# Kernel tuning notes

Hardware: AMD Instinct MI355X
Metric: run time of the kernel (lower is better)

Reference implementation:

```python
import jax, jax.numpy as jnp
import numpy as np

B, H, W = 4, 112, 112
N = H * W              # 12544 tokens
NBHD = 48              # local neighborhood size
DIM = 256
OUT_DIM = 512
INNER = 4              # inner_ch of weight_net
TABLE = 4096           # pre_table rows
ALPHA = 4.0
DS_RATE = 0.25
STRIDE = 2
RESERVE = (H // 4) * (W // 4)  # 784 reserve tokens (pos % 4 == 0)
EPS = 1e-5


def _ln(x, g, b):
    m = x.mean(-1, keepdims=True)
    v = ((x - m) ** 2).mean(-1, keepdims=True)
    return (x - m) / jnp.sqrt(v + EPS) * g + b


def setup_inputs() -> dict:
    key = jax.random.key(0)
    ks = jax.random.split(key, 8)
    ii, jj = jnp.meshgrid(jnp.arange(H), jnp.arange(W), indexing='ij')
    pos = jnp.stack([ii, jj], -1).reshape(1, N, 2).astype(jnp.float32)
    pos = jnp.tile(pos, (B, 1, 1))                             # b x n x 2 integer grid
    feat = jax.random.normal(ks[0], (B, N, DIM), jnp.float32)
    member_idx = jax.random.randint(ks[1], (B, N, NBHD), 0, N)
    cluster_mask = (jax.random.uniform(ks[2], (B, N, NBHD)) > 0.1).astype(jnp.float32)
    learned_prob = jax.random.uniform(ks[3], (B, N, 1), dtype=jnp.float32)
    pe_idx = jax.random.randint(ks[4], (B, N, NBHD), 0, TABLE)
    pre_table = jax.random.normal(ks[5], (TABLE, 5), jnp.float32)
    w1 = jax.random.normal(ks[6], (5, INNER), jnp.float32) * 0.4
    b1 = jnp.zeros((INNER,), jnp.float32)
    ln1_g = jnp.ones((INNER,), jnp.float32)
    ln1_b = jnp.zeros((INNER,), jnp.float32)
    norm_g = jnp.ones((INNER * DIM,), jnp.float32)
    norm_b = jnp.zeros((INNER * DIM,), jnp.float32)
    lin_w = jax.random.normal(ks[7], (INNER * DIM, OUT_DIM), jnp.float32) * (1.0 / np.sqrt(INNER * DIM))
    lin_b = jnp.zeros((OUT_DIM,), jnp.float32)
    return dict(pos=pos, feat=feat, member_idx=member_idx, cluster_mask=cluster_mask,
                learned_prob=learned_prob, stride=STRIDE, pe_idx=pe_idx, reserve_num=RESERVE,
                pre_table=pre_table, w1=w1, b1=b1, ln1_g=ln1_g, ln1_b=ln1_b,
                norm_g=norm_g, norm_b=norm_b, lin_w=lin_w, lin_b=lin_b)


def reference(pos, feat, member_idx, cluster_mask, learned_prob, stride, pe_idx,
              reserve_num, pre_table, w1, b1, ln1_g, ln1_b, norm_g, norm_b, lin_w, lin_b):
    b, n, c = feat.shape
    keep_num = int(n * DS_RATE)
    pos_long = pos.astype(jnp.int32)
    # stride == 2 branch: tokens on the coarse grid get prob 1
    grid_prob = jnp.all(pos_long % stride == 0, axis=-1).astype(jnp.float32)      # b x n
    lp_s = jax.lax.stop_gradient(learned_prob).reshape(b, n) * ALPHA              # detached scores
    final_prob = grid_prob + lp_s
    reserve_mask = jnp.all(pos_long % (stride * 2) == 0, axis=-1).astype(jnp.float32)
    final_prob = final_prob + reserve_mask * (-100.0)
    sample_num = keep_num - reserve_num
    _, sample_idx = jax.lax.top_k(final_prob, sample_num)                         # b x sample_num
    # per-row nonzero of reserve_mask (exactly reserve_num hits per row)
    flat_nz = jnp.nonzero(reserve_mask.reshape(-1) > 0, size=b * reserve_num)[0]
    reserve_idx = (flat_nz % n).reshape(b, reserve_num).astype(sample_idx.dtype)
    idx = jnp.concatenate([sample_idx, reserve_idx], axis=1)                      # b x keep_num

    pos_k = jnp.take_along_axis(pos, idx[:, :, None], axis=1)                     # b x keep x 2
    nbhd = member_idx.shape[-1]
    mem_k = jnp.take_along_axis(member_idx, idx[:, :, None], axis=1)              # b x keep x nbhd
    pe_k = jnp.take_along_axis(pe_idx, idx[:, :, None], axis=1)
    cm_k = jnp.take_along_axis(cluster_mask, idx[:, :, None], axis=1)
    lp = jnp.take_along_axis(learned_prob, mem_k.reshape(b, -1, 1), axis=1)
    lp = lp.reshape(b, keep_num, nbhd, 1)

    # weight_net on the small PE table, then gather per-edge weights
    wt = jax.nn.gelu(_ln(pre_table @ w1 + b1, ln1_g, ln1_b), approximate=False)   # TABLE x INNER
    weights = wt[pe_k]                                                            # b x keep x nbhd x INNER
    weights = weights * (lp * cm_k[..., None])

    # CLUSTENWF: gather neighbor features and weighted-sum over the neighborhood
    gathered = jnp.take_along_axis(feat, mem_k.reshape(b, -1, 1), axis=1)
    gathered = gathered.reshape(b, keep_num, nbhd, c)                             # b x keep x nbhd x c
    out = jnp.einsum('bnkm,bnkc->bnmc', weights, gathered).reshape(b, keep_num, INNER * c)
    out = _ln(out, norm_g, norm_b)
    return pos_k, out @ lin_w + lin_b
```

## Files before the change

### kernel.cpp

```cpp
#include <hip/hip_runtime.h>

typedef unsigned short u16;
typedef unsigned int u32;
typedef unsigned long long u64;

#define NB 4
#define NTOK 12544
#define NBHD 48
#define DIM 256
#define OUTD 512
#define KEEPN 3136
#define SAMPLEN 2352
#define RESN 784
#define GW 112
#define TABLE 4096
#define POSN (NB * KEEPN * 2)
#define QTR (NTOK / 4)
#define NBKT 16384

#define BLKM 128
#define BLKN 256
#define BROW 40

#define FEATB_BYTES (25690112ull)
#define XWS_BYTES   (25690112ull)
#define LINT_BYTES  (1048576ull)
#define KEYS_BYTES  (401408ull)
#define PART_BYTES  (802816ull)
#define WS_NEED (FEATB_BYTES + XWS_BYTES + LINT_BYTES + KEYS_BYTES + PART_BYTES)

__device__ __forceinline__ float bf2f(u16 u) {
    union { u32 i; float f; } v; v.i = ((u32)u) << 16; return v.f;
}
__device__ __forceinline__ float asf(u32 u) {
    union { u32 i; float f; } v; v.i = u; return v.f;
}
__device__ __forceinline__ u16 f2bf(float f) {
    union { u32 i; float f; } v; v.f = f;
    return (u16)((v.i + 0x7FFFu + ((v.i >> 16) & 1u)) >> 16);
}

typedef __bf16 bf16x8 __attribute__((ext_vector_type(8)));
typedef float floatx4 __attribute__((ext_vector_type(4)));
typedef float floatx2 __attribute__((ext_vector_type(2)));

__device__ __forceinline__ float make_f(float lp, int n) {
    int i = n / GW, j = n % GW;
    float f = lp * 4.0f;
    if (((i | j) & 1) == 0) f = 1.0f + f;
    if (((i | j) & 3) == 0) f = f + (-100.0f);
    return f;
}
__device__ __forceinline__ u64 f_to_key(float f, int n) {
    union { float f; u32 u; } v; v.f = f;
    u32 m = (v.u & 0x80000000u) ? ~v.u : (v.u | 0x80000000u);
    return (((u64)m) << 32) | (u64)(0xFFFFFFFFu - (u32)n);
}
__device__ __forceinline__ int f_to_bucket(float f) {
    int b = (int)floorf(f * 3276.8f);
    return b < 0 ? 0 : (b > NBKT - 1 ? NBKT - 1 : b);
}

__global__ __launch_bounds__(256) void prep_kernel(
    const float* __restrict__ feat, u16* __restrict__ featb,
    const float* __restrict__ lin_w, u16* __restrict__ linT,
    u32* __restrict__ hist,
    const float* __restrict__ pre_table, const float* __restrict__ w1,
    const float* __restrict__ b1, const float* __restrict__ g1,
    const float* __restrict__ bb1, float* __restrict__ wt) {
    __shared__ u16 T[64 * 65];
    int bid = blockIdx.x;
    int t = threadIdx.x;
    if (bid >= 128) {
        int ft = (bid - 128) * 256 + t;
        float4 v = ((const float4*)feat)[ft];
        u64 w = (u64)f2bf(v.x) | ((u64)f2bf(v.y) << 16) |
                ((u64)f2bf(v.z) << 32) | ((u64)f2bf(v.w) << 48);
        ((u64*)featb)[ft] = w;
        return;
    }
    int bx = bid & 15, by = bid >> 4;
    int k0 = bx * 64, n0 = by * 64;
    hist[bid * 512 + t] = 0;
    hist[bid * 512 + 256 + t] = 0;
    int gid = bid * 256 + t;
    if (gid < TABLE) {
        float z[4];
#pragma unroll
        for (int m = 0; m < 4; ++m) {
            float acc = b1[m];
#pragma unroll
            for (int d = 0; d < 5; ++d) acc += pre_table[gid * 5 + d] * w1[d * 4 + m];
            z[m] = acc;
        }
        float mean = (z[0] + z[1] + z[2] + z[3]) * 0.25f;
        float var = 0.0f;
#pragma unroll
        for (int m = 0; m < 4; ++m) { float d = z[m] - mean; var += d * d; }
        float rstd = rsqrtf(var * 0.25f + 1e-5f);
        float wv[4];
#pragma unroll
        for (int m = 0; m < 4; ++m) {
            float y = (z[m] - mean) * rstd * g1[m] + bb1[m];
            wv[m] = 0.5f * y * (1.0f + erff(y * 0.70710678118654752f));
        }
        *(float4*)&wt[gid * 4] = make_float4(wv[0], wv[1], wv[2], wv[3]);
    }
    int r = t >> 2, c4 = (t & 3) * 16;
#pragma unroll
    for (int i = 0; i < 4; ++i) {
        float4 v = *(const float4*)&lin_w[(size_t)(k0 + r) * OUTD + n0 + c4 + i * 4];
        T[(c4 + i * 4 + 0) * 65 + r] = f2bf(v.x);
        T[(c4 + i * 4 + 1) * 65 + r] = f2bf(v.y);
        T[(c4 + i * 4 + 2) * 65 + r] = f2bf(v.z);
        T[(c4 + i * 4 + 3) * 65 + r] = f2bf(v.w);
    }
    __syncthreads();
    int nl = t >> 2, kc = (t & 3) * 16;
    union { uint4 v[2]; u16 h[16]; } u;
#pragma unroll
    for (int i = 0; i < 16; ++i) u.h[i] = T[nl * 65 + kc + i];
    u16* dst = &linT[(size_t)(n0 + nl) * 1024 + k0 + kc];
    *(uint4*)(dst + 0) = u.v[0];
    *(uint4*)(dst + 8) = u.v[1];
}

__global__ __launch_bounds__(256) void hist_kernel(
    const float* __restrict__ lprob, u32* __restrict__ hist) {
    int g = blockIdx.x * 256 + threadIdx.x;
    int b = g / NTOK, n = g % NTOK;
    int bkt = f_to_bucket(make_f(lprob[g], n));
    atomicAdd(&hist[b * NBKT + bkt], 1u);
}

__global__ __launch_bounds__(1024) void prefix_kernel(
    const u32* __restrict__ hist, u32* __restrict__ base, u32* __restrict__ cursor) {
    int b = blockIdx.x, t = threadIdx.x;
    const u32* h = hist + b * NBKT;
    u32 loc[16], own = 0;
#pragma unroll
    for (int i = 0; i < 16; ++i) { loc[i] = h[t * 16 + i]; own += loc[i]; }
    __shared__ u32 buf[2][1024];
    buf[0][t] = own;
    __syncthreads();
    int src = 0;
    for (int off = 1; off < 1024; off <<= 1) {
        u32 v = buf[src][t] + ((t + off < 1024) ? buf[src][t + off] : 0u);
        buf[src ^ 1][t] = v;
        src ^= 1;
        __syncthreads();
    }
    u32 above = buf[src][t] - own;
    u32 suf = 0, bout[16];
    for (int i = 15; i >= 0; --i) { bout[i] = above + suf; suf += loc[i]; }
    u32* bb = base + b * NBKT;
    u32* cc = cursor + b * NBKT;
#pragma unroll
    for (int i = 0; i < 16; ++i) { bb[t * 16 + i] = bout[i]; cc[t * 16 + i] = bout[i]; }
}

__global__ __launch_bounds__(256) void scatter_kernel(
    const float* __restrict__ lprob, u32* __restrict__ cursor,
    u64* __restrict__ slots) {
    int g = blockIdx.x * 256 + threadIdx.x;
    int b = g / NTOK, n = g % NTOK;
    float f = make_f(lprob[g], n);
    int bkt = f_to_bucket(f);
    u32 s = atomicAdd(&cursor[b * NBKT + bkt], 1u);
    slots[b * NTOK + s] = f_to_key(f, n);
}

__global__ __launch_bounds__(256) void rank_finalize_kernel(
    const float* __restrict__ lprob, const u32* __restrict__ hist,
    const u32* __restrict__ base, const u64* __restrict__ slots,
    float* __restrict__ pos_out) {
    int g = blockIdx.x * 256 + threadIdx.x;
    int b = g / NTOK, n = g % NTOK;
    int i = n / GW, j = n % GW;
    if (((i | j) & 3) == 0) {
        int r = (i >> 2) * 28 + (j >> 2);
        int slot = b * KEEPN + SAMPLEN + r;
        pos_out[slot * 2 + 0] = (float)i;
        pos_out[slot * 2 + 1] = (float)j;
        return;
    }
    float f = make_f(lprob[g], n);
    int bkt = f_to_bucket(f);
    u32 r0 = base[b * NBKT + bkt];
    if (r0 >= SAMPLEN) return;
    u64 my = f_to_key(f, n);
    u32 cnt = hist[b * NBKT + bkt];
    const u64* sl = slots + b * NTOK + r0;
    u32 rank = r0;
    for (u32 s = 0; s < cnt; ++s) rank += (sl[s] > my) ? 1u : 0u;
    if (rank < SAMPLEN) {
        int slot = b * KEEPN + (int)rank;
        pos_out[slot * 2 + 0] = (float)i;
        pos_out[slot * 2 + 1] = (float)j;
    }
}

__device__ __forceinline__ void consume8(uint2 d, float4 w,
                                         floatx2* accA, floatx2* accB) {
    floatx2 w01 = {w.x, w.y};
    floatx2 w23 = {w.z, w.w};
    float c0 = asf(d.x << 16);
    float c1 = asf(d.x & 0xFFFF0000u);
    float c2 = asf(d.y << 16);
    float c3 = asf(d.y & 0xFFFF0000u);
    floatx2 c0v = {c0, c0}, c1v = {c1, c1}, c2v = {c2, c2}, c3v = {c3, c3};
    accA[0] = __builtin_elementwise_fma(w01, c0v, accA[0]);
    accB[0] = __builtin_elementwise_fma(w23, c0v, accB[0]);
    accA[1] = __builtin_elementwise_fma(w01, c1v, accA[1]);
    accB[1] = __builtin_elementwise_fma(w23, c1v, accB[1]);
    accA[2] = __builtin_elementwise_fma(w01, c2v, accA[2]);
    accB[2] = __builtin_elementwise_fma(w23, c2v, accB[2]);
    accA[3] = __builtin_elementwise_fma(w01, c3v, accA[3]);
    accB[3] = __builtin_elementwise_fma(w23, c3v, accB[3]);
}

__global__ __launch_bounds__(256) void token_v8_kernel(
    const float* __restrict__ pos_in, u16* __restrict__ xdst,
    const int* __restrict__ member_idx, const int* __restrict__ pe_idx,
    const float* __restrict__ cmask, const float* __restrict__ lprob,
    const u16* __restrict__ featb, const float* __restrict__ wt,
    const float* __restrict__ norm_g, const float* __restrict__ norm_b) {
    int bi = blockIdx.x;
    int xcd = bi & 7, jj = bi >> 3;
    int b = xcd >> 1;
    int tid = threadIdx.x;
    int wave = tid >> 6, lane = tid & 63;
    int t = b * KEEPN + (xcd & 1) * 1568 + jj * 4 + wave;

    __shared__ float4 w_s[4][NBHD];

    float2 pp = *(const float2*)&pos_in[t * 2];
    int n_src = (int)pp.x * GW + (int)pp.y;

    u32 moffb = 0;
    if (lane < NBHD) {
        int e = (b * NTOK + n_src) * NBHD + lane;
        int mem = member_idx[e];
        float sc = lprob[b * NTOK + mem] * cmask[e];
        float4 w4 = *(const float4*)&wt[pe_idx[e] * 4];
        w_s[wave][lane] = make_float4(w4.x * sc, w4.y * sc, w4.z * sc, w4.w * sc);
        moffb = (u32)mem * (DIM * 2);
    }
    __syncthreads();

    floatx2 accA[4] = {};
    floatx2 accB[4] = {};
    const char* fb = (const char*)featb + (size_t)b * NTOK * DIM * 2;
    u32 lane8 = (u32)lane * 8;

#define GLD(dst, kk) { u32 mk = (u32)__builtin_amdgcn_readlane((int)moffb, (kk)); \
                       dst = *(const uint2*)(fb + mk + lane8); }
#pragma unroll
    for (int kb = 0; kb < NBHD; kb += 8) {
        uint2 d0, d1, d2, d3, d4, d5, d6, d7;
        GLD(d0, kb + 0); GLD(d1, kb + 1); GLD(d2, kb + 2); GLD(d3, kb + 3);
        GLD(d4, kb + 4); GLD(d5, kb + 5); GLD(d6, kb + 6); GLD(d7, kb + 7);
        consume8(d0, w_s[wave][kb + 0], accA, accB);
        consume8(d1, w_s[wave][kb + 1], accA, accB);
        consume8(d2, w_s[wave][kb + 2], accA, accB);
        consume8(d3, w_s[wave][kb + 3], accA, accB);
        consume8(d4, w_s[wave][kb + 4], accA, accB);
        consume8(d5, w_s[wave][kb + 5], accA, accB);
        consume8(d6, w_s[wave][kb + 6], accA, accB);
        consume8(d7, w_s[wave][kb + 7], accA, accB);
    }
#undef GLD

    float s1 = 0.0f, s2 = 0.0f;
#pragma unroll
    for (int j = 0; j < 4; ++j) {
        float v0 = accA[j][0], v1 = accA[j][1], v2 = accB[j][0], v3 = accB[j][1];
        s1 += v0 + v1 + v2 + v3;
        s2 += v0 * v0 + v1 * v1 + v2 * v2 + v3 * v3;
    }
#pragma unroll
    for (int off = 32; off > 0; off >>= 1) {
        s1 += __shfl_xor(s1, off, 64);
        s2 += __shfl_xor(s2, off, 64);
    }
    float mean = s1 * (1.0f / 1024.0f);
    float var = fmaxf(s2 * (1.0f / 1024.0f) - mean * mean, 0.0f);
    float rstd = rsqrtf(var + 1e-5f);

    u16* Xp = xdst + (size_t)t * 1024;
#pragma unroll
    for (int m = 0; m < 4; ++m) {
        int cc = m * 256 + lane * 4;
        float4 g4 = *(const float4*)&norm_g[cc];
        float4 b4 = *(const float4*)&norm_b[cc];
        float v0 = (m == 0) ? accA[0][0] : (m == 1) ? accA[0][1]
                 : (m == 2) ? accB[0][0] : accB[0][1];
        float v1 = (m == 0) ? accA[1][0] : (m == 1) ? accA[1][1]
                 : (m == 2) ? accB[1][0] : accB[1][1];
        float v2 = (m == 0) ? accA[2][0] : (m == 1) ? accA[2][1]
                 : (m == 2) ? accB[2][0] : accB[2][1];
        float v3 = (m == 0) ? accA[3][0] : (m == 1) ? accA[3][1]
                 : (m == 2) ? accB[3][0] : accB[3][1];
        u16 h0 = f2bf((v0 - mean) * rstd * g4.x + b4.x);
        u16 h1 = f2bf((v1 - mean) * rstd * g4.y + b4.y);
        u16 h2 = f2bf((v2 - mean) * rstd * g4.z + b4.z);
        u16 h3 = f2bf((v3 - mean) * rstd * g4.w + b4.w);
        u64 w = (u64)h0 | ((u64)h1 << 16) | ((u64)h2 << 32) | ((u64)h3 << 48);
        *(u64*)(Xp + cc) = w;
    }
}

#define GROW 40
__global__ __launch_bounds__(256) void gemm_tile_kernel(
    const u16* __restrict__ xws, const u16* __restrict__ linT,
    const float* __restrict__ lin_b, float* __restrict__ out) {
    __shared__ __align__(16) u16 As[128 * GROW];
    __shared__ __align__(16) u16 Bs[64 * GROW];
    int bid = blockIdx.x;
    int xcd = bid & 7, c = bid >> 3;
    int tile = xcd * 98 + c;
    int m0 = (tile >> 3) * 128, n0 = (tile & 7) * 64;

    int tid = threadIdx.x;
    int wave = tid >> 6, lane = tid & 63;
    int l15 = lane & 15, quad = lane >> 4;
    int wm = wave >> 1, wn = wave & 1;
    int sr = tid >> 2, sk = (tid & 3) * 8;

    const u16* Ap0 = xws + (size_t)(m0 + sr) * 1024 + sk;
    const u16* Ap1 = Ap0 + (size_t)64 * 1024;
    const u16* Bp0 = linT + (size_t)(n0 + sr) * 1024 + sk;

    uint4 a0 = *(const uint4*)(Ap0);
    uint4 a1 = *(const uint4*)(Ap1);
    uint4 b0 = *(const uint4*)(Bp0);

    floatx4 acc[4][2] = {};
    for (int kk = 0; kk < 1024; kk += 32) {
        __syncthreads();
        *(uint4*)&As[sr * GROW + sk] = a0;
        *(uint4*)&As[(64 + sr) * GROW + sk] = a1;
        *(uint4*)&Bs[sr * GROW + sk] = b0;
        __syncthreads();
        if (kk + 32 < 1024) {
            a0 = *(const uint4*)(Ap0 + kk + 32);
            a1 = *(const uint4*)(Ap1 + kk + 32);
            b0 = *(const uint4*)(Bp0 + kk + 32);
        }
        bf16x8 af[4], bfv[2];
#pragma unroll
        for (int mi = 0; mi < 4; ++mi)
            af[mi] = *(const bf16x8*)&As[(wm * 64 + mi * 16 + l15) * GROW + quad * 8];
#pragma unroll
        for (int ni = 0; ni < 2; ++ni)
            bfv[ni] = *(const bf16x8*)&Bs[(wn * 32 + ni * 16 + l15) * GROW + quad * 8];
#pragma unroll
        for (int mi = 0; mi < 4; ++mi)
#pragma unroll
            for (int ni = 0; ni < 2; ++ni)
                acc[mi][ni] = __builtin_amdgcn_mfma_f32_16x16x32_bf16(
                    af[mi], bfv[ni], acc[mi][ni], 0, 0, 0);
    }
#pragma unroll
    for (int ni = 0; ni < 2; ++ni) {
        int col = n0 + wn * 32 + ni * 16 + l15;
        float bias = lin_b[col];
#pragma unroll
        for (int mi = 0; mi < 4; ++mi)
#pragma unroll
            for (int reg = 0; reg < 4; ++reg) {
                int row = m0 + wm * 64 + mi * 16 + quad * 4 + reg;
                out[(size_t)row * OUTD + col] = acc[mi][ni][reg] + bias;
            }
    }
}

__global__ __launch_bounds__(256) void key_kernel(
    const float* __restrict__ lprob, u64* __restrict__ keys) {
    int g = blockIdx.x * 256 + threadIdx.x;
    int n = g % NTOK;
    keys[g] = f_to_key(make_f(lprob[g], n), n);
}

__global__ __launch_bounds__(256) void partial_rank_kernel(
    const u64* __restrict__ keys, u32* __restrict__ part) {
    int b = blockIdx.y, z = blockIdx.z;
    int n = blockIdx.x * 256 + threadIdx.x;
    u64 my = keys[b * NTOK + n];
    const u64* kb = keys + b * NTOK + z * QTR;
    u32 cnt = 0;
    for (int t = 0; t < QTR; t += 8) {
#pragma unroll
        for (int j = 0; j < 8; ++j) cnt += (kb[t + j] > my) ? 1u : 0u;
    }
    part[(z * NB + b) * NTOK + n] = cnt;
}

__global__ __launch_bounds__(256) void finalize_kernel(
    const u32* __restrict__ part, float* __restrict__ pos_out) {
    int b = blockIdx.y;
    int n = blockIdx.x * 256 + threadIdx.x;
    int g = b * NTOK + n;
    u32 rank = part[g] + part[(NB + b) * NTOK + n] +
               part[(2 * NB + b) * NTOK + n] + part[(3 * NB + b) * NTOK + n];
    int i = n / GW, j = n % GW;
    if (rank < SAMPLEN) {
        int slot = b * KEEPN + (int)rank;
        pos_out[slot * 2 + 0] = (float)i;
        pos_out[slot * 2 + 1] = (float)j;
    }
    if (((i | j) & 3) == 0) {
        int r = (i >> 2) * 28 + (j >> 2);
        int slot = b * KEEPN + SAMPLEN + r;
        pos_out[slot * 2 + 0] = (float)i;
        pos_out[slot * 2 + 1] = (float)j;
    }
}

__global__ __launch_bounds__(256) void token_fb_kernel(
    const float* __restrict__ pos_in, u16* __restrict__ xdst,
    const int* __restrict__ member_idx, const int* __restrict__ pe_idx,
    const float* __restrict__ cmask, const float* __restrict__ lprob,
    const float* __restrict__ featf, const float* __restrict__ pre_table,
    const float* __restrict__ w1, const float* __restrict__ b1,
    const float* __restrict__ g1, const float* __restrict__ bb1,
    const float* __restrict__ norm_g, const float* __restrict__ norm_b) {
    int t = blockIdx.x;
    int b = t / KEEPN;
    int tid = threadIdx.x;
    __shared__ int mem_s[NBHD];
    __shared__ float4 w_s[NBHD];
    __shared__ float red[10];

    int n_src = (int)pos_in[t * 2 + 0] * GW + (int)pos_in[t * 2 + 1];

    if (tid < NBHD) {
        int e = (b * NTOK + n_src) * NBHD + tid;
        int mem = member_idx[e];
        int pe = pe_idx[e];
        float cm = cmask[e];
        float lpe = lprob[b * NTOK + mem];
        float z[4];
#pragma unroll
        for (int m = 0; m < 4; ++m) {
            float acc = b1[m];
#pragma unroll
            for (int d = 0; d < 5; ++d) acc += pre_table[pe * 5 + d] * w1[d * 4 + m];
            z[m] = acc;
        }
        float mean = (z[0] + z[1] + z[2] + z[3]) * 0.25f;
        float var = 0.0f;
#pragma unroll
        for (int m = 0; m < 4; ++m) { float d = z[m] - mean; var += d * d; }
        float rstd = rsqrtf(var * 0.25f + 1e-5f);
        float sc = lpe * cm;
        float wv[4];
#pragma unroll
        for (int m = 0; m < 4; ++m) {
            float y = (z[m] - mean) * rstd * g1[m] + bb1[m];
            wv[m] = 0.5f * y * (1.0f + erff(y * 0.70710678118654752f)) * sc;
        }
        w_s[tid] = make_float4(wv[0], wv[1], wv[2], wv[3]);
        mem_s[tid] = mem;
    }
    __syncthreads();

    float a0 = 0.f, a1 = 0.f, a2 = 0.f, a3 = 0.f;
    size_t base = (size_t)b * NTOK * DIM + tid;
#pragma unroll 8
    for (int k = 0; k < NBHD; ++k) {
        float g = featf[base + (size_t)mem_s[k] * DIM];
        float4 w = w_s[k];
        a0 += w.x * g; a1 += w.y * g; a2 += w.z * g; a3 += w.w * g;
    }
    float s1 = a0 + a1 + a2 + a3;
    float s2 = a0 * a0 + a1 * a1 + a2 * a2 + a3 * a3;
#pragma unroll
    for (int off = 32; off > 0; off >>= 1) {
        s1 += __shfl_down(s1, off, 64);
        s2 += __shfl_down(s2, off, 64);
    }
    int wave = tid >> 6, lane = tid & 63;
    if (lane == 0) { red[wave] = s1; red[4 + wave] = s2; }
    __syncthreads();
    if (tid == 0) {
        float S = red[0] + red[1] + red[2] + red[3];
        float Q = red[4] + red[5] + red[6] + red[7];
        float mean = S * (1.0f / 1024.0f);
        float var = fmaxf(Q * (1.0f / 1024.0f) - mean * mean, 0.0f);
        red[8] = mean; red[9] = rsqrtf(var + 1e-5f);
    }
    __syncthreads();
    float mean = red[8], rstd = red[9];
    float acc4[4] = {a0, a1, a2, a3};
    u16* Xp = xdst + (size_t)t * 1024;
#pragma unroll
    for (int m = 0; m < 4; ++m) {
        int cc = m * 256 + tid;
        float v = (acc4[m] - mean) * rstd * norm_g[cc] + norm_b[cc];
        Xp[cc] = f2bf(v);
    }
}

__global__ __launch_bounds__(256) void gemm_inplace_kernel(
    const float* __restrict__ lin_w, const float* __restrict__ lin_b,
    float* __restrict__ out) {
    __shared__ __align__(16) u16 Bs[BLKN * BROW];
    int tile_m = blockIdx.x;
    int nblk = blockIdx.y;
    int tid = threadIdx.x;
    int wave = tid >> 6, lane = tid & 63;
    int l15 = lane & 15, quad = lane >> 4;

    const u16* Xbase = (const u16*)out;
    floatx4 acc[8][4] = {};

    for (int kk = 0; kk < 1024; kk += 32) {
        __syncthreads();
#pragma unroll
        for (int it = 0; it < 4; ++it) {
            int task = it * 256 + tid;
            int kp = task >> 6;
            int ng = task & 63;
            int k = kp * 2;
            int n0 = nblk * BLKN + ng * 4;
            float4 fa = *(const float4*)&lin_w[(size_t)(kk + k) * OUTD + n0];
            float4 fb = *(const float4*)&lin_w[(size_t)(kk + k + 1) * OUTD + n0];
            u16* bp = &Bs[(ng * 4) * BROW + k];
            *(u32*)(bp + 0 * BROW) = (u32)f2bf(fa.x) | ((u32)f2bf(fb.x) << 16);
            *(u32*)(bp + 1 * BROW) = (u32)f2bf(fa.y) | ((u32)f2bf(fb.y) << 16);
            *(u32*)(bp + 2 * BROW) = (u32)f2bf(fa.z) | ((u32)f2bf(fb.z) << 16);
            *(u32*)(bp + 3 * BROW) = (u32)f2bf(fa.w) | ((u32)f2bf(fb.w) << 16);
        }
        __syncthreads();
        bf16x8 bfrag[4];
#pragma unroll
        for (int ni = 0; ni < 4; ++ni)
            bfrag[ni] = *(const bf16x8*)&Bs[(wave * 64 + ni * 16 + l15) * BROW + quad * 8];
#pragma unroll
        for (int mi = 0; mi < 8; ++mi) {
            int row = tile_m * BLKM + mi * 16 + l15;
            bf16x8 af = *(const bf16x8*)&Xbase[(size_t)row * 1024 + kk + quad * 8];
#pragma unroll
            for (int ni = 0; ni < 4; ++ni)
                acc[mi][ni] = __builtin_amdgcn_mfma_f32_16x16x32_bf16(
                    af, bfrag[ni], acc[mi][ni], 0, 0, 0);
        }
    }
    __syncthreads();
#pragma unroll
    for (int mi = 0; mi < 8; ++mi)
#pragma unroll
        for (int ni = 0; ni < 4; ++ni) {
            int col = nblk * BLKN + wave * 64 + ni * 16 + l15;
            float bias = lin_b[col];
#pragma unroll
            for (int reg = 0; reg < 4; ++reg) {
                int row = tile_m * BLKM + mi * 16 + quad * 4 + reg;
                out[(size_t)row * OUTD + col] = acc[mi][ni][reg] + bias;
            }
        }
}

extern "C" void kernel_launch(void* const* d_in, const int* in_sizes, int n_in,
                              void* d_out, int out_size, void* d_ws, size_t ws_size,
                              hipStream_t stream) {
    const float* feat     = (const float*)d_in[1];
    const int* member_idx = (const int*)d_in[2];
    const float* cmask    = (const float*)d_in[3];
    const float* lprob    = (const float*)d_in[4];
    const int* pe_idx     = (const int*)d_in[6];
    const float* pre_table= (const float*)d_in[8];
    const float* w1       = (const float*)d_in[9];
    const float* b1       = (const float*)d_in[10];
    const float* g1       = (const float*)d_in[11];
    const float* bb1      = (const float*)d_in[12];
    const float* norm_g   = (const float*)d_in[13];
    const float* norm_b   = (const float*)d_in[14];
    const float* lin_w    = (const float*)d_in[15];
    const float* lin_b    = (const float*)d_in[16];

    float* pos_out = (float*)d_out;
    float* out     = pos_out + POSN;

    if (ws_size >= WS_NEED) {
        char* ws = (char*)d_ws;
        u16* featb = (u16*)ws;
        u16* xws   = (u16*)(ws + FEATB_BYTES);
        u16* linT  = (u16*)(ws + FEATB_BYTES + XWS_BYTES);
        u64* slots = (u64*)(ws + FEATB_BYTES + XWS_BYTES + LINT_BYTES);
        u32* hist  = (u32*)(ws + FEATB_BYTES + XWS_BYTES + LINT_BYTES + KEYS_BYTES);
        u32* base  = hist + NB * NBKT;
        u32* curs  = base + NB * NBKT;
        float* wtbuf = out;

        prep_kernel<<<12672, 256, 0, stream>>>(
            feat, featb, lin_w, linT, hist, pre_table, w1, b1, g1, bb1, wtbuf);
        hist_kernel<<<(NB * NTOK) / 256, 256, 0, stream>>>(lprob, hist);
        prefix_kernel<<<NB, 1024, 0, stream>>>(hist, base, curs);
        scatter_kernel<<<(NB * NTOK) / 256, 256, 0, stream>>>(lprob, curs, slots);
        rank_finalize_kernel<<<(NB * NTOK) / 256, 256, 0, stream>>>(
            lprob, hist, base, slots, pos_out);
        token_v8_kernel<<<(NB * KEEPN) / 4, 256, 0, stream>>>(
            pos_out, xws, member_idx, pe_idx, cmask, lprob, featb,
            wtbuf, norm_g, norm_b);
        gemm_tile_kernel<<<784, 256, 0, stream>>>(xws, linT, lin_b, out);
    } else {
        u64* keys = (u64*)out;
        u32* part = (u32*)((char*)out + 401408);

        key_kernel<<<(NB * NTOK) / 256, 256, 0, stream>>>(lprob, keys);
        partial_rank_kernel<<<dim3(49, NB, 4), 256, 0, stream>>>(keys, part);
        finalize_kernel<<<dim3(49, NB), 256, 0, stream>>>(part, pos_out);
        token_fb_kernel<<<NB * KEEPN, 256, 0, stream>>>(
            pos_out, (u16*)out, member_idx, pe_idx, cmask, lprob, feat,
            pre_table, w1, b1, g1, bb1, norm_g, norm_b);
        gemm_inplace_kernel<<<dim3(98, 2), 256, 0, stream>>>(lin_w, lin_b, out);
    }
}
```

Baseline: 238.4 us.

## Split neighborhood across half-waves with 16-byte gathers and LDS offsets

```diff
diff --git a/kernel.cpp b/kernel.cpp
--- a/kernel.cpp
+++ b/kernel.cpp
@@ -200,26 +200,24 @@
     }
 }
 
-__device__ __forceinline__ void consume8(uint2 d, float4 w,
-                                         floatx2* accA, floatx2* accB) {
+__device__ __forceinline__ void consume16(uint4 d, float4 w,
+                                          floatx2* accA, floatx2* accB) {
     floatx2 w01 = {w.x, w.y};
     floatx2 w23 = {w.z, w.w};
-    float c0 = asf(d.x << 16);
-    float c1 = asf(d.x & 0xFFFF0000u);
-    float c2 = asf(d.y << 16);
-    float c3 = asf(d.y & 0xFFFF0000u);
-    floatx2 c0v = {c0, c0}, c1v = {c1, c1}, c2v = {c2, c2}, c3v = {c3, c3};
-    accA[0] = __builtin_elementwise_fma(w01, c0v, accA[0]);
-    accB[0] = __builtin_elementwise_fma(w23, c0v, accB[0]);
-    accA[1] = __builtin_elementwise_fma(w01, c1v, accA[1]);
-    accB[1] = __builtin_elementwise_fma(w23, c1v, accB[1]);
-    accA[2] = __builtin_elementwise_fma(w01, c2v, accA[2]);
-    accB[2] = __builtin_elementwise_fma(w23, c2v, accB[2]);
-    accA[3] = __builtin_elementwise_fma(w01, c3v, accA[3]);
-    accB[3] = __builtin_elementwise_fma(w23, c3v, accB[3]);
-}
-
-__global__ __launch_bounds__(256) void token_v8_kernel(
+    float c[8];
+    c[0] = asf(d.x << 16); c[1] = asf(d.x & 0xFFFF0000u);
+    c[2] = asf(d.y << 16); c[3] = asf(d.y & 0xFFFF0000u);
+    c[4] = asf(d.z << 16); c[5] = asf(d.z & 0xFFFF0000u);
+    c[6] = asf(d.w << 16); c[7] = asf(d.w & 0xFFFF0000u);
+#pragma unroll
+    for (int j = 0; j < 8; ++j) {
+        floatx2 cs = {c[j], c[j]};
+        accA[j] = __builtin_elementwise_fma(w01, cs, accA[j]);
+        accB[j] = __builtin_elementwise_fma(w23, cs, accB[j]);
+    }
+}
+
+__global__ __launch_bounds__(256) void token_v9_kernel(
     const float* __restrict__ pos_in, u16* __restrict__ xdst,
     const int* __restrict__ member_idx, const int* __restrict__ pe_idx,
     const float* __restrict__ cmask, const float* __restrict__ lprob,
@@ -232,48 +230,56 @@
     int wave = tid >> 6, lane = tid & 63;
     int t = b * KEEPN + (xcd & 1) * 1568 + jj * 4 + wave;
 
-    __shared__ float4 w_s[4][NBHD];
+    __shared__ __align__(16) float4 w_s[4][NBHD];
+    __shared__ __align__(16) int moff_s[4][NBHD];
 
     float2 pp = *(const float2*)&pos_in[t * 2];
     int n_src = (int)pp.x * GW + (int)pp.y;
 
-    u32 moffb = 0;
     if (lane < NBHD) {
         int e = (b * NTOK + n_src) * NBHD + lane;
         int mem = member_idx[e];
         float sc = lprob[b * NTOK + mem] * cmask[e];
         float4 w4 = *(const float4*)&wt[pe_idx[e] * 4];
-        w_s[wave][lane] = make_float4(w4.x * sc, w4.y * sc, w4.z * sc, w4.w * sc);
-        moffb = (u32)mem * (DIM * 2);
+        int slot = (lane & 1) * 24 + (lane >> 1);
+        w_s[wave][slot] = make_float4(w4.x * sc, w4.y * sc, w4.z * sc, w4.w * sc);
+        moff_s[wave][slot] = mem * (DIM * 2);
     }
     __syncthreads();
 
-    floatx2 accA[4] = {};
-    floatx2 accB[4] = {};
+    int half = lane >> 5;
+    int l5 = lane & 31;
+    u32 l16 = (u32)l5 * 16;
     const char* fb = (const char*)featb + (size_t)b * NTOK * DIM * 2;
-    u32 lane8 = (u32)lane * 8;
-
-#define GLD(dst, kk) { u32 mk = (u32)__builtin_amdgcn_readlane((int)moffb, (kk)); \
-                       dst = *(const uint2*)(fb + mk + lane8); }
-#pragma unroll
-    for (int kb = 0; kb < NBHD; kb += 8) {
-        uint2 d0, d1, d2, d3, d4, d5, d6, d7;
-        GLD(d0, kb + 0); GLD(d1, kb + 1); GLD(d2, kb + 2); GLD(d3, kb + 3);
-        GLD(d4, kb + 4); GLD(d5, kb + 5); GLD(d6, kb + 6); GLD(d7, kb + 7);
-        consume8(d0, w_s[wave][kb + 0], accA, accB);
-        consume8(d1, w_s[wave][kb + 1], accA, accB);
-        consume8(d2, w_s[wave][kb + 2], accA, accB);
-        consume8(d3, w_s[wave][kb + 3], accA, accB);
-        consume8(d4, w_s[wave][kb + 4], accA, accB);
-        consume8(d5, w_s[wave][kb + 5], accA, accB);
-        consume8(d6, w_s[wave][kb + 6], accA, accB);
-        consume8(d7, w_s[wave][kb + 7], accA, accB);
-    }
-#undef GLD
+    const int* obase = &moff_s[wave][half * 24];
+    const float4* wbase = &w_s[wave][half * 24];
+
+    floatx2 accA[8] = {};
+    floatx2 accB[8] = {};
+#pragma unroll
+    for (int pb = 0; pb < 6; ++pb) {
+        int4 o = *(const int4*)(obase + pb * 4);
+        uint4 e0 = *(const uint4*)(fb + (u32)o.x + l16);
+        uint4 e1 = *(const uint4*)(fb + (u32)o.y + l16);
+        uint4 e2 = *(const uint4*)(fb + (u32)o.z + l16);
+        uint4 e3 = *(const uint4*)(fb + (u32)o.w + l16);
+        consume16(e0, wbase[pb * 4 + 0], accA, accB);
+        consume16(e1, wbase[pb * 4 + 1], accA, accB);
+        consume16(e2, wbase[pb * 4 + 2], accA, accB);
+        consume16(e3, wbase[pb * 4 + 3], accA, accB);
+    }
+
+#pragma unroll
+    for (int j = 0; j < 8; ++j) {
+        accA[j][0] += __shfl_xor(accA[j][0], 32, 64);
+        accA[j][1] += __shfl_xor(accA[j][1], 32, 64);
+        accB[j][0] += __shfl_xor(accB[j][0], 32, 64);
+        accB[j][1] += __shfl_xor(accB[j][1], 32, 64);
+    }
 
     float s1 = 0.0f, s2 = 0.0f;
 #pragma unroll
-    for (int j = 0; j < 4; ++j) {
+    for (int j = 0; j < 8; ++j) {
         float v0 = accA[j][0], v1 = accA[j][1], v2 = accB[j][0], v3 = accB[j][1];
         s1 += v0 + v1 + v2 + v3;
         s2 += v0 * v0 + v1 * v1 + v2 * v2 + v3 * v3;
@@ -283,30 +289,42 @@
         s1 += __shfl_xor(s1, off, 64);
         s2 += __shfl_xor(s2, off, 64);
     }
-    float mean = s1 * (1.0f / 1024.0f);
-    float var = fmaxf(s2 * (1.0f / 1024.0f) - mean * mean, 0.0f);
+    float mean = s1 * (1.0f / 2048.0f);
+    float var = fmaxf(s2 * (1.0f / 2048.0f) - mean * mean, 0.0f);
     float rstd = rsqrtf(var + 1e-5f);
 
     u16* Xp = xdst + (size_t)t * 1024;
-#pragma unroll
-    for (int m = 0; m < 4; ++m) {
-        int cc = m * 256 + lane * 4;
-        float4 g4 = *(const float4*)&norm_g[cc];
-        float4 b4 = *(const float4*)&norm_b[cc];
-        float v0 = (m == 0) ? accA[0][0] : (m == 1) ? accA[0][1]
-                 : (m == 2) ? accB[0][0] : accB[0][1];
-        float v1 = (m == 0) ? accA[1][0] : (m == 1) ? accA[1][1]
-                 : (m == 2) ? accB[1][0] : accB[1][1];
-        float v2 = (m == 0) ? accA[2][0] : (m == 1) ? accA[2][1]
-                 : (m == 2) ? accB[2][0] : accB[2][1];
-        float v3 = (m == 0) ? accA[3][0] : (m == 1) ? accA[3][1]
-                 : (m == 2) ? accB[3][0] : accB[3][1];
-        u16 h0 = f2bf((v0 - mean) * rstd * g4.x + b4.x);
-        u16 h1 = f2bf((v1 - mean) * rstd * g4.y + b4.y);
-        u16 h2 = f2bf((v2 - mean) * rstd * g4.z + b4.z);
-        u16 h3 = f2bf((v3 - mean) * rstd * g4.w + b4.w);
-        u64 w = (u64)h0 | ((u64)h1 << 16) | ((u64)h2 << 32) | ((u64)h3 << 48);
-        *(u64*)(Xp + cc) = w;
+    int cc0 = (half * 2) * 256 + l5 * 8;
+    {
+        float4 g0 = *(const float4*)&norm_g[cc0];
+        float4 g1 = *(const float4*)&norm_g[cc0 + 4];
+        float4 b0 = *(const float4*)&norm_b[cc0];
+        float4 b1 = *(const float4*)&norm_b[cc0 + 4];
+        float ga[8] = {g0.x, g0.y, g0.z, g0.w, g1.x, g1.y, g1.z, g1.w};
+        float ba[8] = {b0.x, b0.y, b0.z, b0.w, b1.x, b1.y, b1.z, b1.w};
+        union { uint4 v; u16 h[8]; } pk;
+#pragma unroll
+        for (int j = 0; j < 8; ++j) {
+            float v = half ? accB[j][0] : accA[j][0];
+            pk.h[j] = f2bf((v - mean) * rstd * ga[j] + ba[j]);
+        }
+        *(uint4*)(Xp + cc0) = pk.v;
+    }
+    {
+        int cc1 = cc0 + 256;
+        float4 g0 = *(const float4*)&norm_g[cc1];
+        float4 g1 = *(const float4*)&norm_g[cc1 + 4];
+        float4 b0 = *(const float4*)&norm_b[cc1];
+        float4 b1 = *(const float4*)&norm_b[cc1 + 4];
+        float ga[8] = {g0.x, g0.y, g0.z, g0.w, g1.x, g1.y, g1.z, g1.w};
+        float ba[8] = {b0.x, b0.y, b0.z, b0.w, b1.x, b1.y, b1.z, b1.w};
+        union { uint4 v; u16 h[8]; } pk;
+#pragma unroll
+        for (int j = 0; j < 8; ++j) {
+            float v = half ? accB[j][1] : accA[j][1];
+            pk.h[j] = f2bf((v - mean) * rstd * ga[j] + ba[j]);
+        }
+        *(uint4*)(Xp + cc1) = pk.v;
     }
 }
 
@@ -601,7 +619,7 @@
         scatter_kernel<<<(NB * NTOK) / 256, 256, 0, stream>>>(lprob, curs, slots);
         rank_finalize_kernel<<<(NB * NTOK) / 256, 256, 0, stream>>>(
             lprob, hist, base, slots, pos_out);
-        token_v8_kernel<<<(NB * KEEPN) / 4, 256, 0, stream>>>(
+        token_v9_kernel<<<(NB * KEEPN) / 4, 256, 0, stream>>>(
             pos_out, xws, member_idx, pe_idx, cmask, lprob, featb,
             wtbuf, norm_g, norm_b);
         gemm_tile_kernel<<<784, 256, 0, stream>>>(xws, linT, lin_b, out);
```

New measurement: 237.6 us. No clear change (-0.4%).
